# Optimization experiments

Measured on AMD Instinct MI355X. Metric: run time of the kernel, lower is better.

## Reference

```python
import jax, jax.numpy as jnp
import numpy as np

WEIGHT = 0.01

def setup_inputs() -> dict:
    key = jax.random.key(0)
    k1, k2 = jax.random.split(key)
    shape = jax.random.normal(k1, (16, 4096, 3), dtype=jnp.float32)
    template = jax.random.normal(k2, (16, 4096, 3), dtype=jnp.float32)
    return {"shape": shape, "template": template}

def _chamfer(pred, target):
    # Euclidean cdist via the |x|^2 + |y|^2 - 2<x,y> expansion to avoid a (B,M,N,3) tensor.
    p2 = jnp.sum(pred * pred, axis=-1)          # (B, M)
    t2 = jnp.sum(target * target, axis=-1)      # (B, N)
    cross = jnp.einsum('bmd,bnd->bmn', pred, target)  # (B, M, N)
    d2 = p2[:, :, None] + t2[None if p2.ndim == 1 else slice(None), None, :] - 2.0 * cross
    dist = jnp.sqrt(jnp.maximum(d2, 0.0))       # (B, M, N) euclidean, matches torch.cdist
    min_p2t = jnp.min(dist, axis=2)             # (B, M)
    min_t2p = jnp.min(dist, axis=1)             # (B, N)
    chamfer = jnp.sum(min_p2t, axis=1) + jnp.sum(min_t2p, axis=1)  # (B,)
    return jnp.mean(chamfer)                    # reduction='mean'

def reference(shape, template):
    return WEIGHT * _chamfer(shape, template)
```

## Files before the change

kernel.cpp:

```cpp
#include <hip/hip_runtime.h>

#define NPTS 4096
#define NBATCH 16
#define THREADS 256
#define QPB 256
#define TCH 1024
#define NCH (NPTS / TCH)
#define REC 24

typedef __attribute__((ext_vector_type(8))) short short8;
typedef __attribute__((ext_vector_type(4))) float float4v;

static __device__ __forceinline__ unsigned short f2bf(float f) {
  unsigned int u = __builtin_bit_cast(unsigned int, f);
  u = (u + 0x7FFFu + ((u >> 16) & 1u)) >> 16;
  return (unsigned short)u;
}
static __device__ __forceinline__ float bf2f(unsigned short h) {
  unsigned int u = ((unsigned int)h) << 16;
  return __builtin_bit_cast(float, u);
}

__global__ __launch_bounds__(THREADS, 2) void chamfer_mfma(
    const float* __restrict__ shape, const float* __restrict__ tmpl,
    float* __restrict__ out) {
  __shared__ unsigned short tgt[TCH * REC];
  __shared__ unsigned short qry[QPB * REC];
  __shared__ float p2s[QPB];
  __shared__ float redbuf[4];

  const int qc = blockIdx.x;
  const int b = blockIdx.y;
  const int dir = blockIdx.z;
  const float* Pb = (dir == 0 ? shape : tmpl) + (size_t)b * NPTS * 3;
  const float* Tb = (dir == 0 ? tmpl : shape) + (size_t)b * NPTS * 3;

  const int tid = threadIdx.x;
  const int lane = tid & 63;
  const int wave = tid >> 6;
  const int quad = lane >> 4;
  const int n15 = lane & 15;
  const bool kactive = (quad < 2);

  {
    const int qg = qc * QPB + tid;
    const float px = Pb[3 * qg + 0], py = Pb[3 * qg + 1], pz = Pb[3 * qg + 2];
    const float ux = -2.0f * px, uy = -2.0f * py, uz = -2.0f * pz;
    const unsigned short hx = f2bf(ux), hy = f2bf(uy), hz = f2bf(uz);
    const unsigned short lx = f2bf(ux - bf2f(hx)), ly = f2bf(uy - bf2f(hy)),
                         lz = f2bf(uz - bf2f(hz));
    const unsigned short ONE = 0x3F80;
    short8 v0, v1;
    v0[0] = hx; v0[1] = hx; v0[2] = lx; v0[3] = hy;
    v0[4] = hy; v0[5] = ly; v0[6] = hz; v0[7] = hz;
    v1[0] = lz; v1[1] = ONE; v1[2] = ONE; v1[3] = 0;
    v1[4] = 0;  v1[5] = 0;  v1[6] = 0;  v1[7] = 0;
    *(short8*)&qry[tid * REC] = v0;
    *(short8*)&qry[tid * REC + 8] = v1;
    p2s[tid] = fmaf(px, px, fmaf(py, py, pz * pz));
  }
  __syncthreads();

  short8 af[4];
  #pragma unroll
  for (int t = 0; t < 4; ++t) {
    const int q = (wave * 4 + t) * 16 + n15;
    short8 v = {};
    if (kactive) v = *(const short8*)&qry[q * REC + quad * 8];
    af[t] = v;
  }

  const float INF = 3.402823466e38f;
  float4v mins[4];
  #pragma unroll
  for (int t = 0; t < 4; ++t) mins[t] = (float4v){INF, INF, INF, INF};
  const float4v zero4 = {0.0f, 0.0f, 0.0f, 0.0f};

  const float4* T4 = (const float4*)Tb;
  for (int ch = 0; ch < NCH; ++ch) {
    __syncthreads();
    {
      const int g = ch * (TCH / 4) + tid;
      const float4 a = T4[g * 3 + 0];
      const float4 c = T4[g * 3 + 1];
      const float4 d = T4[g * 3 + 2];
      const float X[4] = {a.x, a.w, c.z, d.y};
      const float Y[4] = {a.y, c.x, c.w, d.z};
      const float Z[4] = {a.z, c.y, d.x, d.w};
      #pragma unroll
      for (int p = 0; p < 4; ++p) {
        const float x = X[p], y = Y[p], z = Z[p];
        const float t2 = fmaf(x, x, fmaf(y, y, z * z));
        const unsigned short hx = f2bf(x), hy = f2bf(y), hz = f2bf(z);
        const unsigned short lx = f2bf(x - bf2f(hx)), ly = f2bf(y - bf2f(hy)),
                             lz = f2bf(z - bf2f(hz));
        const unsigned short h2 = f2bf(t2), l2 = f2bf(t2 - bf2f(h2));
        short8 v0, v1;
        v0[0] = hx; v0[1] = lx; v0[2] = hx; v0[3] = hy;
        v0[4] = ly; v0[5] = hy; v0[6] = hz; v0[7] = lz;
        v1[0] = hz; v1[1] = h2; v1[2] = l2; v1[3] = 0;
        v1[4] = 0;  v1[5] = 0;  v1[6] = 0;  v1[7] = 0;
        unsigned short* dst = &tgt[(tid * 4 + p) * REC];
        *(short8*)dst = v0;
        *(short8*)(dst + 8) = v1;
      }
    }
    __syncthreads();

    const unsigned short* bbase = &tgt[n15 * REC + quad * 8];
    #pragma unroll 4
    for (int tn = 0; tn < TCH / 16; ++tn) {
      short8 bf = {};
      if (kactive) bf = *(const short8*)(bbase + tn * (16 * REC));
      #pragma unroll
      for (int t = 0; t < 4; ++t) {
        float4v d2 = __builtin_amdgcn_mfma_f32_16x16x32_bf16(af[t], bf, zero4, 0, 0, 0);
        mins[t].x = fminf(mins[t].x, d2.x);
        mins[t].y = fminf(mins[t].y, d2.y);
        mins[t].z = fminf(mins[t].z, d2.z);
        mins[t].w = fminf(mins[t].w, d2.w);
      }
    }
  }

  #pragma unroll
  for (int t = 0; t < 4; ++t) {
    #pragma unroll
    for (int m = 1; m <= 8; m <<= 1) {
      mins[t].x = fminf(mins[t].x, __shfl_xor(mins[t].x, m, 64));
      mins[t].y = fminf(mins[t].y, __shfl_xor(mins[t].y, m, 64));
      mins[t].z = fminf(mins[t].z, __shfl_xor(mins[t].z, m, 64));
      mins[t].w = fminf(mins[t].w, __shfl_xor(mins[t].w, m, 64));
    }
  }

  float s = 0.0f;
  if (n15 == 0) {
    #pragma unroll
    for (int t = 0; t < 4; ++t) {
      const int qb = (wave * 4 + t) * 16 + quad * 4;
      s += sqrtf(fmaxf(mins[t].x + p2s[qb + 0], 0.0f));
      s += sqrtf(fmaxf(mins[t].y + p2s[qb + 1], 0.0f));
      s += sqrtf(fmaxf(mins[t].z + p2s[qb + 2], 0.0f));
      s += sqrtf(fmaxf(mins[t].w + p2s[qb + 3], 0.0f));
    }
  }
  s += __shfl_xor(s, 16, 64);
  s += __shfl_xor(s, 32, 64);
  if (lane == 0) redbuf[wave] = s;
  __syncthreads();
  if (tid == 0) {
    atomicAdd(out, (redbuf[0] + redbuf[1] + redbuf[2] + redbuf[3]) * (0.01f / 16.0f));
  }
}

extern "C" void kernel_launch(void* const* d_in, const int* in_sizes, int n_in,
                              void* d_out, int out_size, void* d_ws, size_t ws_size,
                              hipStream_t stream) {
  const float* shape = (const float*)d_in[0];
  const float* tmpl = (const float*)d_in[1];
  float* out = (float*)d_out;

  hipMemsetAsync(out, 0, sizeof(float) * out_size, stream);

  dim3 grid(NPTS / QPB, NBATCH, 2);
  chamfer_mfma<<<grid, dim3(THREADS), 0, stream>>>(shape, tmpl, out);
}
```

Measured before the change: 91.04 us.

## Switch to 32x32x16 bf16 MFMA with a 2x2 register tile and swizzled LDS

Replaces the 16x16x32 MFMA, where half the lanes fed zero K-data, with 32x32x16 MFMA. The K=16 packing now matches the 11 used coefficients, so no lanes idle on K. Each wave computes a 2x2 block of 32x32 tiles, reusing each A and B fragment twice and folding pairs of results in the min before accumulating. The target LDS records shrink from 24 to 16 shorts and use an XOR swizzle to avoid bank conflicts. The cost is 32 float accumulators per thread plus 64 temporary MFMA outputs, which raises register pressure, and occupancy is pinned through waves_per_eu.

```diff
diff --git a/kernel.cpp b/kernel.cpp
--- a/kernel.cpp
+++ b/kernel.cpp
@@ -6,10 +6,9 @@
 #define QPB 256
 #define TCH 1024
 #define NCH (NPTS / TCH)
-#define REC 24
 
 typedef __attribute__((ext_vector_type(8))) short short8;
-typedef __attribute__((ext_vector_type(4))) float float4v;
+typedef __attribute__((ext_vector_type(16))) float float16v;
 
 static __device__ __forceinline__ unsigned short f2bf(float f) {
   unsigned int u = __builtin_bit_cast(unsigned int, f);
@@ -20,12 +19,17 @@
   unsigned int u = ((unsigned int)h) << 16;
   return __builtin_bit_cast(float, u);
 }
+static __device__ __forceinline__ int toff(int j, int h) {
+  return (j * 16 + h * 8) ^ (((j >> 2) & 7) << 3);
+}
 
-__global__ __launch_bounds__(THREADS, 2) void chamfer_mfma(
-    const float* __restrict__ shape, const float* __restrict__ tmpl,
-    float* __restrict__ out) {
-  __shared__ unsigned short tgt[TCH * REC];
-  __shared__ unsigned short qry[QPB * REC];
+__global__ __launch_bounds__(THREADS)
+__attribute__((amdgpu_waves_per_eu(2, 2)))
+void chamfer_mfma(const float* __restrict__ shape,
+                  const float* __restrict__ tmpl,
+                  float* __restrict__ out) {
+  __shared__ unsigned short tgt[TCH * 16];
+  __shared__ unsigned short qry[QPB * 16];
   __shared__ float p2s[QPB];
   __shared__ float redbuf[4];
 
@@ -38,9 +42,8 @@
   const int tid = threadIdx.x;
   const int lane = tid & 63;
   const int wave = tid >> 6;
-  const int quad = lane >> 4;
-  const int n15 = lane & 15;
-  const bool kactive = (quad < 2);
+  const int n = lane & 31;
+  const int kg = lane >> 5;
 
   {
     const int qg = qc * QPB + tid;
@@ -55,26 +58,19 @@
     v0[4] = hy; v0[5] = ly; v0[6] = hz; v0[7] = hz;
     v1[0] = lz; v1[1] = ONE; v1[2] = ONE; v1[3] = 0;
     v1[4] = 0;  v1[5] = 0;  v1[6] = 0;  v1[7] = 0;
-    *(short8*)&qry[tid * REC] = v0;
-    *(short8*)&qry[tid * REC + 8] = v1;
+    *(short8*)&qry[tid * 16] = v0;
+    *(short8*)&qry[tid * 16 + 8] = v1;
     p2s[tid] = fmaf(px, px, fmaf(py, py, pz * pz));
   }
   __syncthreads();
 
-  short8 af[4];
-  #pragma unroll
-  for (int t = 0; t < 4; ++t) {
-    const int q = (wave * 4 + t) * 16 + n15;
-    short8 v = {};
-    if (kactive) v = *(const short8*)&qry[q * REC + quad * 8];
-    af[t] = v;
-  }
+  const short8 af0 = *(const short8*)&qry[(wave * 64 + n) * 16 + kg * 8];
+  const short8 af1 = *(const short8*)&qry[(wave * 64 + 32 + n) * 16 + kg * 8];
 
   const float INF = 3.402823466e38f;
-  float4v mins[4];
+  float acc0[16], acc1[16];
   #pragma unroll
-  for (int t = 0; t < 4; ++t) mins[t] = (float4v){INF, INF, INF, INF};
-  const float4v zero4 = {0.0f, 0.0f, 0.0f, 0.0f};
+  for (int r = 0; r < 16; ++r) { acc0[r] = INF; acc1[r] = INF; }
 
   const float4* T4 = (const float4*)Tb;
   for (int ch = 0; ch < NCH; ++ch) {
@@ -100,52 +96,49 @@
         v0[4] = ly; v0[5] = hy; v0[6] = hz; v0[7] = lz;
         v1[0] = hz; v1[1] = h2; v1[2] = l2; v1[3] = 0;
         v1[4] = 0;  v1[5] = 0;  v1[6] = 0;  v1[7] = 0;
-        unsigned short* dst = &tgt[(tid * 4 + p) * REC];
-        *(short8*)dst = v0;
-        *(short8*)(dst + 8) = v1;
+        const int j = tid * 4 + p;
+        *(short8*)&tgt[toff(j, 0)] = v0;
+        *(short8*)&tgt[toff(j, 1)] = v1;
       }
     }
     __syncthreads();
 
-    const unsigned short* bbase = &tgt[n15 * REC + quad * 8];
-    #pragma unroll 4
-    for (int tn = 0; tn < TCH / 16; ++tn) {
-      short8 bf = {};
-      if (kactive) bf = *(const short8*)(bbase + tn * (16 * REC));
+    for (int tp = 0; tp < TCH / 64; ++tp) {
+      const short8 b0 = *(const short8*)&tgt[toff(tp * 64 + n, kg)];
+      const short8 b1 = *(const short8*)&tgt[toff(tp * 64 + 32 + n, kg)];
+      const float16v z = {};
+      float16v d00 = __builtin_amdgcn_mfma_f32_32x32x16_bf16(af0, b0, z, 0, 0, 0);
+      float16v d10 = __builtin_amdgcn_mfma_f32_32x32x16_bf16(af1, b0, z, 0, 0, 0);
+      float16v d01 = __builtin_amdgcn_mfma_f32_32x32x16_bf16(af0, b1, z, 0, 0, 0);
+      float16v d11 = __builtin_amdgcn_mfma_f32_32x32x16_bf16(af1, b1, z, 0, 0, 0);
       #pragma unroll
-      for (int t = 0; t < 4; ++t) {
-        float4v d2 = __builtin_amdgcn_mfma_f32_16x16x32_bf16(af[t], bf, zero4, 0, 0, 0);
-        mins[t].x = fminf(mins[t].x, d2.x);
-        mins[t].y = fminf(mins[t].y, d2.y);
-        mins[t].z = fminf(mins[t].z, d2.z);
-        mins[t].w = fminf(mins[t].w, d2.w);
-      }
+      for (int r = 0; r < 16; ++r)
+        acc0[r] = fminf(fminf(d00[r], d01[r]), acc0[r]);
+      #pragma unroll
+      for (int r = 0; r < 16; ++r)
+        acc1[r] = fminf(fminf(d10[r], d11[r]), acc1[r]);
     }
   }
 
   #pragma unroll
-  for (int t = 0; t < 4; ++t) {
+  for (int m = 1; m <= 16; m <<= 1) {
     #pragma unroll
-    for (int m = 1; m <= 8; m <<= 1) {
-      mins[t].x = fminf(mins[t].x, __shfl_xor(mins[t].x, m, 64));
-      mins[t].y = fminf(mins[t].y, __shfl_xor(mins[t].y, m, 64));
-      mins[t].z = fminf(mins[t].z, __shfl_xor(mins[t].z, m, 64));
-      mins[t].w = fminf(mins[t].w, __shfl_xor(mins[t].w, m, 64));
+    for (int r = 0; r < 16; ++r) {
+      acc0[r] = fminf(acc0[r], __shfl_xor(acc0[r], m, 64));
+      acc1[r] = fminf(acc1[r], __shfl_xor(acc1[r], m, 64));
     }
   }
 
   float s = 0.0f;
-  if (n15 == 0) {
+  if (n == 0) {
+    const int qb = wave * 64;
     #pragma unroll
-    for (int t = 0; t < 4; ++t) {
-      const int qb = (wave * 4 + t) * 16 + quad * 4;
-      s += sqrtf(fmaxf(mins[t].x + p2s[qb + 0], 0.0f));
-      s += sqrtf(fmaxf(mins[t].y + p2s[qb + 1], 0.0f));
-      s += sqrtf(fmaxf(mins[t].z + p2s[qb + 2], 0.0f));
-      s += sqrtf(fmaxf(mins[t].w + p2s[qb + 3], 0.0f));
+    for (int r = 0; r < 16; ++r) {
+      const int row = (r & 3) + 8 * (r >> 2) + 4 * kg;
+      s += sqrtf(fmaxf(acc0[r] + p2s[qb + row], 0.0f));
+      s += sqrtf(fmaxf(acc1[r] + p2s[qb + 32 + row], 0.0f));
     }
   }
-  s += __shfl_xor(s, 16, 64);
   s += __shfl_xor(s, 32, 64);
   if (lane == 0) redbuf[wave] = s;
   __syncthreads();
```

Result: faster. 81.88 us (-10.1%).
